# Optimization experiments

Hardware: AMD Instinct MI355X
Metric: run time of the kernel (lower is better)

## Reference

```python
import jax, jax.numpy as jnp
import numpy as np

LN_EPS = 1e-5

def setup_inputs() -> dict:
    key = jax.random.key(0)
    ks = jax.random.split(key, 12)
    B, S, M, C, D = 16, 1024, 4096, 768, 256
    inp = {
        'seed_xyz_norm': jax.random.normal(ks[0], (B, S, 3), jnp.float32),
        'p_last': jax.random.normal(ks[1], (B, M, 3), jnp.float32),
        'f_last': jax.random.normal(ks[2], (B, C, M), jnp.float32),
        'seed_features': jax.random.normal(ks[3], (B, D, S), jnp.float32),
        # LayerNorm params over C
        'ln_gamma': jnp.ones((C,), jnp.float32),
        'ln_beta': jnp.zeros((C,), jnp.float32),
        # conv1d projector C -> 256 (kernel size 1) + ReLU
        'proj_w': jax.random.normal(ks[4], (D, C), jnp.float32) * (1.0 / np.sqrt(C)),
        'proj_b': jnp.zeros((D,), jnp.float32),
        # fusion MLP: concat512 -> 512 -> 256 (1x1 convs)
        'mlp_w1': jax.random.normal(ks[5], (2 * D, 2 * D), jnp.float32) * (1.0 / np.sqrt(2 * D)),
        'mlp_b1': jnp.zeros((2 * D,), jnp.float32),
        'mlp_w2': jax.random.normal(ks[6], (D, 2 * D), jnp.float32) * (1.0 / np.sqrt(2 * D)),
        'mlp_b2': jnp.zeros((D,), jnp.float32),
    }
    return inp


def reference(seed_xyz_norm, p_last, f_last, seed_features,
              ln_gamma, ln_beta, proj_w, proj_b,
              mlp_w1, mlp_b1, mlp_w2, mlp_b2):
    # --- nearest_neighbor_gather_features ---
    # squared distance [B,S,M]; argmin over M, gather features [B,C,S]
    d2 = jnp.sum(seed_xyz_norm * seed_xyz_norm, -1, keepdims=True) \
         - 2.0 * jnp.einsum('bsd,bmd->bsm', seed_xyz_norm, p_last) \
         + jnp.sum(p_last * p_last, -1)[:, None, :]
    idx = jnp.argmin(d2, axis=-1)                                   # [B,S]
    lift3d_raw = jnp.take_along_axis(f_last, idx[:, None, :], axis=2)  # [B,C,S]

    # --- LayerNorm over channel dim C ---
    mu = jnp.mean(lift3d_raw, axis=1, keepdims=True)
    var = jnp.mean((lift3d_raw - mu) ** 2, axis=1, keepdims=True)
    x_ln = (lift3d_raw - mu) * jax.lax.rsqrt(var + LN_EPS)
    x_ln = x_ln * ln_gamma[None, :, None] + ln_beta[None, :, None]

    # --- conv1d projector (1x1) + ReLU ---
    proj = jax.nn.relu(jnp.einsum('oc,bcs->bos', proj_w, x_ln) + proj_b[None, :, None])

    # --- concat fusion MLP ---
    fused = jnp.concatenate([seed_features, proj], axis=1)          # [B,512,S]
    h = jax.nn.relu(jnp.einsum('oc,bcs->bos', mlp_w1, fused) + mlp_b1[None, :, None])
    mixed = jnp.einsum('oc,bcs->bos', mlp_w2, h) + mlp_b2[None, :, None]  # [B,256,S]
    return mixed
```

## Files before the change

### kernel.cpp

```cpp
#include <hip/hip_runtime.h>

namespace {

constexpr int B = 16, S = 1024, M = 4096, C = 768, D = 256;

typedef __attribute__((ext_vector_type(8))) short bf16x8;
typedef __attribute__((ext_vector_type(4))) float f32x4;

__device__ inline ushort f2bf(float f) {
  uint u = __float_as_uint(f);
  uint r = (u + 0x7FFFu + ((u >> 16) & 1u)) >> 16;
  return (ushort)r;
}

__global__ __launch_bounds__(256)
void nn_kernel(const float* __restrict__ xyz, const float* __restrict__ p,
               int* __restrict__ idx_out) {
  const int b = blockIdx.y;
  const int t = threadIdx.x;
  const int seed = blockIdx.x * 16 + (t >> 4);
  const int l16 = t & 15;

  const float sx = xyz[((size_t)b * S + seed) * 3 + 0];
  const float sy = xyz[((size_t)b * S + seed) * 3 + 1];
  const float sz = xyz[((size_t)b * S + seed) * 3 + 2];
  const float ss = __fadd_rn(__fadd_rn(__fmul_rn(sx, sx), __fmul_rn(sy, sy)),
                             __fmul_rn(sz, sz));

  __shared__ float4 pt[256];

  float best = 3.4028235e38f;
  int besti = 0;
  const float* pb = p + (size_t)b * M * 3;

  for (int m0 = 0; m0 < M; m0 += 256) {
    __syncthreads();
    {
      const float a0 = pb[(size_t)(m0 + t) * 3 + 0];
      const float a1 = pb[(size_t)(m0 + t) * 3 + 1];
      const float a2 = pb[(size_t)(m0 + t) * 3 + 2];
      const float pp = __fadd_rn(__fadd_rn(__fmul_rn(a0, a0), __fmul_rn(a1, a1)),
                                 __fmul_rn(a2, a2));
      pt[t] = make_float4(a0, a1, a2, pp);
    }
    __syncthreads();
    #pragma unroll 4
    for (int j = l16; j < 256; j += 16) {
      const float4 q = pt[j];
      float dot = __fmul_rn(sx, q.x);
      dot = __fadd_rn(dot, __fmul_rn(sy, q.y));
      dot = __fadd_rn(dot, __fmul_rn(sz, q.z));
      const float d2 = __fadd_rn(__fsub_rn(ss, __fmul_rn(2.0f, dot)), q.w);
      const int mi = m0 + j;
      if (d2 < best || (d2 == best && mi < besti)) { best = d2; besti = mi; }
    }
  }
  #pragma unroll
  for (int off = 8; off >= 1; off >>= 1) {
    const float ob = __shfl_xor(best, off, 16);
    const int   oi = __shfl_xor(besti, off, 16);
    if (ob < best || (ob == best && oi < besti)) { best = ob; besti = oi; }
  }
  if (l16 == 0) idx_out[b * S + seed] = besti;
}

__global__ __launch_bounds__(256)
void bucket_sort_kernel(const int* __restrict__ idx, int* __restrict__ sIdx,
                        int* __restrict__ sS) {
  const int b = blockIdx.x;
  const int t = threadIdx.x;
  __shared__ int keys[1024];
  __shared__ int cnt[256];
  __shared__ int base[256];
  __shared__ int wsum[4];

  cnt[t] = 0;
  #pragma unroll
  for (int i = 0; i < 4; ++i) keys[t + 256 * i] = idx[b * S + t + 256 * i];
  __syncthreads();
  #pragma unroll
  for (int i = 0; i < 4; ++i) atomicAdd(&cnt[keys[t + 256 * i] >> 4], 1);
  __syncthreads();

  const int v = cnt[t];
  int sc = v;
  #pragma unroll
  for (int off = 1; off < 64; off <<= 1) {
    const int o = __shfl_up(sc, off);
    if ((t & 63) >= off) sc += o;
  }
  if ((t & 63) == 63) wsum[t >> 6] = sc;
  __syncthreads();
  int wb = 0;
  #pragma unroll
  for (int w = 0; w < 4; ++w)
    if (w < (t >> 6)) wb += wsum[w];
  base[t] = wb + sc - v;
  cnt[t] = 0;
  __syncthreads();

  #pragma unroll
  for (int i = 0; i < 4; ++i) {
    const int s = t + 256 * i;
    const int m = keys[s];
    const int bu = m >> 4;
    const int r = base[bu] + atomicAdd(&cnt[bu], 1);
    sIdx[b * S + r] = m;
    sS[b * S + r] = s;
  }
}

__global__ __launch_bounds__(256)
void gather_ln_kernel(const float* __restrict__ f, const int* __restrict__ sIdx,
                      const int* __restrict__ sS,
                      const float* __restrict__ gamma, const float* __restrict__ beta,
                      ushort* __restrict__ xln) {
  const int b = blockIdx.y;
  const int rl = blockIdx.x;
  const int r0 = (((rl & 7) << 5) + (rl >> 3)) << 2;
  const int t = threadIdx.x;

  int sR[4], mR[4];
  #pragma unroll
  for (int i = 0; i < 4; ++i) {
    sR[i] = sS[b * S + r0 + i];
    mR[i] = sIdx[b * S + r0 + i];
  }

  const float* fb = f + (size_t)b * C * M;
  float v[4][3];
  #pragma unroll
  for (int i = 0; i < 4; ++i) {
    v[i][0] = fb[(size_t)(t      ) * M + mR[i]];
    v[i][1] = fb[(size_t)(t + 256) * M + mR[i]];
    v[i][2] = fb[(size_t)(t + 512) * M + mR[i]];
  }

  const float g0 = gamma[t], g1 = gamma[t + 256], g2 = gamma[t + 512];
  const float e0 = beta[t],  e1 = beta[t + 256],  e2 = beta[t + 512];

  __shared__ float red[4][4];
  __shared__ float stats[8];
  const int wave = t >> 6;

  float ps[4];
  #pragma unroll
  for (int i = 0; i < 4; ++i) ps[i] = v[i][0] + v[i][1] + v[i][2];
  #pragma unroll
  for (int off = 32; off >= 1; off >>= 1) {
    #pragma unroll
    for (int i = 0; i < 4; ++i) ps[i] += __shfl_xor(ps[i], off);
  }
  if ((t & 63) == 0) {
    #pragma unroll
    for (int i = 0; i < 4; ++i) red[i][wave] = ps[i];
  }
  __syncthreads();
  if (t < 4)
    stats[t] = (red[t][0] + red[t][1] + red[t][2] + red[t][3]) * (1.0f / 768.0f);
  __syncthreads();

  float d[4][3];
  #pragma unroll
  for (int i = 0; i < 4; ++i) {
    const float mu = stats[i];
    d[i][0] = v[i][0] - mu; d[i][1] = v[i][1] - mu; d[i][2] = v[i][2] - mu;
  }
  float pv[4];
  #pragma unroll
  for (int i = 0; i < 4; ++i)
    pv[i] = d[i][0] * d[i][0] + d[i][1] * d[i][1] + d[i][2] * d[i][2];
  #pragma unroll
  for (int off = 32; off >= 1; off >>= 1) {
    #pragma unroll
    for (int i = 0; i < 4; ++i) pv[i] += __shfl_xor(pv[i], off);
  }
  if ((t & 63) == 0) {
    #pragma unroll
    for (int i = 0; i < 4; ++i) red[i][wave] = pv[i];
  }
  __syncthreads();
  if (t < 4) {
    const float var = (red[t][0] + red[t][1] + red[t][2] + red[t][3]) * (1.0f / 768.0f);
    stats[4 + t] = 1.0f / sqrtf(var + 1e-5f);
  }
  __syncthreads();

  #pragma unroll
  for (int i = 0; i < 4; ++i) {
    const float rs = stats[4 + i];
    ushort* o = xln + ((size_t)b * S + sR[i]) * C;
    o[t      ] = f2bf((d[i][0] * rs) * g0 + e0);
    o[t + 256] = f2bf((d[i][1] * rs) * g1 + e1);
    o[t + 512] = f2bf((d[i][2] * rs) * g2 + e2);
  }
}

__global__ __launch_bounds__(256)
void prep_kernel(const float* __restrict__ sf, ushort* __restrict__ fused,
                 const float* __restrict__ w0, int n0, ushort* __restrict__ o0,
                 const float* __restrict__ w1, int n1, ushort* __restrict__ o1,
                 const float* __restrict__ w2, int n2, ushort* __restrict__ o2) {
  __shared__ float tile[64][68];
  const int bid = blockIdx.x;
  const int t = threadIdx.x;

  if (bid < 1024) {
    const int b  = bid >> 6;
    const int d0 = ((bid >> 4) & 3) * 64;
    const int s0 = (bid & 15) * 64;

    const float* inb = sf + ((size_t)b * D + d0) * S + s0;
    #pragma unroll
    for (int q = 0; q < 4; ++q) {
      const int rr = (t >> 4) + q * 16;
      const int c4 = (t & 15) * 4;
      const float4 v = *(const float4*)&inb[(size_t)rr * S + c4];
      *(float4*)&tile[rr][c4] = v;
    }
    __syncthreads();
    #pragma unroll
    for (int q = 0; q < 4; ++q) {
      const int srow = (t >> 4) + q * 16;
      const int dc = (t & 15) * 4;
      ushort4 o;
      o.x = f2bf(tile[dc + 0][srow]);
      o.y = f2bf(tile[dc + 1][srow]);
      o.z = f2bf(tile[dc + 2][srow]);
      o.w = f2bf(tile[dc + 3][srow]);
      *(ushort4*)&fused[((size_t)b * S + s0 + srow) * 512 + d0 + dc] = o;
    }
  } else {
    const int id = bid - 1024;
    const int which = id >> 8;
    const float* src = which == 0 ? w0 : which == 1 ? w1 : w2;
    ushort* dst = which == 0 ? o0 : which == 1 ? o1 : o2;
    const int n = which == 0 ? n0 : which == 1 ? n1 : n2;
    const int i = ((id & 255) * 256 + t) * 4;
    if (i < n) {
      const float4 v = *(const float4*)&src[i];
      ushort4 o;
      o.x = f2bf(v.x); o.y = f2bf(v.y); o.z = f2bf(v.z); o.w = f2bf(v.w);
      *(ushort4*)&dst[i] = o;
    }
  }
}

__global__ __launch_bounds__(256)
void gemm_bf16_kernel(const ushort* __restrict__ W, int K, int O,
                      const ushort* __restrict__ X,
                      const float* __restrict__ bias,
                      void* __restrict__ out, int outMode, int ldOut, int colOff,
                      int relu) {
  const int b  = blockIdx.z;
  const int s0 = blockIdx.x * 128;
  const int o0 = blockIdx.y * 128;
  const int t  = threadIdx.x;
  const int wave = t >> 6;
  const int lane = t & 63;
  const int l16 = lane & 15;
  const int quad = lane >> 4;

  __shared__ ushort Wt[2][128 * 40];
  __shared__ ushort Xt[2][128 * 40];
  __shared__ float biasS[128];

  if (t < 128) biasS[t] = bias[o0 + t];

  f32x4 acc[8][2];
  const f32x4 z = {0.f, 0.f, 0.f, 0.f};
  #pragma unroll
  for (int of = 0; of < 8; ++of) { acc[of][0] = z; acc[of][1] = z; }

  const ushort* Xb = X + (size_t)b * S * K;
  const int kg = t & 3;
  const int row = t >> 2;
  const size_t wBase = (size_t)(o0 + row) * K + kg * 8;
  const size_t xBase = (size_t)(s0 + row) * K + kg * 8;
  const size_t wBase2 = wBase + (size_t)64 * K;
  const size_t xBase2 = xBase + (size_t)64 * K;
  const int T = K >> 5;

  uint4 wv0 = *(const uint4*)&W[wBase];
  uint4 wv1 = *(const uint4*)&W[wBase2];
  uint4 xv0 = *(const uint4*)&Xb[xBase];
  uint4 xv1 = *(const uint4*)&Xb[xBase2];
  *(uint4*)&Wt[0][row * 40 + kg * 8] = wv0;
  *(uint4*)&Wt[0][(row + 64) * 40 + kg * 8] = wv1;
  *(uint4*)&Xt[0][row * 40 + kg * 8] = xv0;
  *(uint4*)&Xt[0][(row + 64) * 40 + kg * 8] = xv1;
  if (T > 1) {
    wv0 = *(const uint4*)&W[wBase + 32];
    wv1 = *(const uint4*)&W[wBase2 + 32];
    xv0 = *(const uint4*)&Xb[xBase + 32];
    xv1 = *(const uint4*)&Xb[xBase2 + 32];
  }
  __syncthreads();

  for (int tt = 0; tt < T; ++tt) {
    const int cur = tt & 1;

    if (tt + 1 < T) {
      *(uint4*)&Wt[cur ^ 1][row * 40 + kg * 8] = wv0;
      *(uint4*)&Wt[cur ^ 1][(row + 64) * 40 + kg * 8] = wv1;
      *(uint4*)&Xt[cur ^ 1][row * 40 + kg * 8] = xv0;
      *(uint4*)&Xt[cur ^ 1][(row + 64) * 40 + kg * 8] = xv1;
    }
    if (tt + 2 < T) {
      const int c = (tt + 2) * 32;
      wv0 = *(const uint4*)&W[wBase + c];
      wv1 = *(const uint4*)&W[wBase2 + c];
      xv0 = *(const uint4*)&Xb[xBase + c];
      xv1 = *(const uint4*)&Xb[xBase2 + c];
    }
    bf16x8 bfr[2];
    #pragma unroll
    for (int sf = 0; sf < 2; ++sf)
      bfr[sf] = *(const bf16x8*)&Xt[cur][(wave * 32 + sf * 16 + l16) * 40 + quad * 8];
    #pragma unroll
    for (int of = 0; of < 8; ++of) {
      const bf16x8 afr = *(const bf16x8*)&Wt[cur][(of * 16 + l16) * 40 + quad * 8];
      acc[of][0] = __builtin_amdgcn_mfma_f32_16x16x32_bf16(afr, bfr[0], acc[of][0], 0, 0, 0);
      acc[of][1] = __builtin_amdgcn_mfma_f32_16x16x32_bf16(afr, bfr[1], acc[of][1], 0, 0, 0);
    }
    __syncthreads();
  }

  if (outMode == 0) {
    ushort* ob = (ushort*)out;
    #pragma unroll
    for (int of = 0; of < 8; ++of) {
      #pragma unroll
      for (int sf = 0; sf < 2; ++sf) {
        const int s = s0 + wave * 32 + sf * 16 + l16;
        const int ol = of * 16 + quad * 4;
        float v0 = acc[of][sf].x + biasS[ol + 0];
        float v1 = acc[of][sf].y + biasS[ol + 1];
        float v2 = acc[of][sf].z + biasS[ol + 2];
        float v3 = acc[of][sf].w + biasS[ol + 3];
        if (relu) {
          v0 = fmaxf(v0, 0.f); v1 = fmaxf(v1, 0.f);
          v2 = fmaxf(v2, 0.f); v3 = fmaxf(v3, 0.f);
        }
        ushort4 st;
        st.x = f2bf(v0); st.y = f2bf(v1); st.z = f2bf(v2); st.w = f2bf(v3);
        *(ushort4*)&ob[((size_t)b * S + s) * ldOut + colOff + o0 + ol] = st;
      }
    }
  } else {
    float* o32 = (float*)out;
    #pragma unroll
    for (int of = 0; of < 8; ++of) {
      #pragma unroll
      for (int sf = 0; sf < 2; ++sf) {
        const int s = s0 + wave * 32 + sf * 16 + l16;
        const int ol = of * 16 + quad * 4;
        const float vr[4] = {acc[of][sf].x, acc[of][sf].y, acc[of][sf].z, acc[of][sf].w};
        #pragma unroll
        for (int r = 0; r < 4; ++r) {
          const int o = o0 + ol + r;
          o32[((size_t)b * O + o) * S + s] = vr[r] + biasS[ol + r];
        }
      }
    }
  }
}

}

extern "C" void kernel_launch(void* const* d_in, const int* in_sizes, int n_in,
                              void* d_out, int out_size, void* d_ws, size_t ws_size,
                              hipStream_t stream) {
  const float* seed_xyz  = (const float*)d_in[0];
  const float* p_last    = (const float*)d_in[1];
  const float* f_last    = (const float*)d_in[2];
  const float* seed_feat = (const float*)d_in[3];
  const float* ln_gamma  = (const float*)d_in[4];
  const float* ln_beta   = (const float*)d_in[5];
  const float* proj_w    = (const float*)d_in[6];
  const float* proj_b    = (const float*)d_in[7];
  const float* mlp_w1    = (const float*)d_in[8];
  const float* mlp_b1    = (const float*)d_in[9];
  const float* mlp_w2    = (const float*)d_in[10];
  const float* mlp_b2    = (const float*)d_in[11];
  float* out = (float*)d_out;

  char* ws = (char*)d_ws;
  int*    idx   = (int*)(ws);
  int*    sIdx  = (int*)(ws + (64 << 10));
  int*    sS    = (int*)(ws + (128 << 10));
  ushort* wp_bf = (ushort*)(ws + (256 << 10));
  ushort* w1_bf = (ushort*)(ws + (640 << 10));
  ushort* w2_bf = (ushort*)(ws + (1152 << 10));
  ushort* xln   = (ushort*)(ws + (2ull << 20));
  ushort* fused = (ushort*)(ws + (26ull << 20));
  ushort* hbuf  = (ushort*)(ws + (42ull << 20));

  nn_kernel<<<dim3(S / 16, B), 256, 0, stream>>>(seed_xyz, p_last, idx);
  bucket_sort_kernel<<<dim3(B), 256, 0, stream>>>(idx, sIdx, sS);

  gather_ln_kernel<<<dim3(S / 4, B), 256, 0, stream>>>(f_last, sIdx, sS,
                                                       ln_gamma, ln_beta, xln);

  prep_kernel<<<dim3(1024 + 768), 256, 0, stream>>>(
      seed_feat, fused,
      proj_w, D * C, wp_bf, mlp_w1, 512 * 512, w1_bf, mlp_w2, 256 * 512, w2_bf);

  gemm_bf16_kernel<<<dim3(S / 128, 256 / 128, B), 256, 0, stream>>>(
      wp_bf, C, 256, xln, proj_b, fused, 0, 512, 256, 1);

  gemm_bf16_kernel<<<dim3(S / 128, 512 / 128, B), 256, 0, stream>>>(
      w1_bf, 512, 512, fused, mlp_b1, hbuf, 0, 512, 0, 1);

  gemm_bf16_kernel<<<dim3(S / 128, 256 / 128, B), 256, 0, stream>>>(
      w2_bf, 512, 256, hbuf, mlp_b2, out, 1, 0, 0, 0);
}
```

Measured before the change: 409.1 us.

## Reshape GEMM tiles to 256x64 with single-buffered LDS staging

Changes the bf16 GEMM block tile from 128 outputs x 128 seeds to 256 outputs x 64 seeds, with each wave owning 16 seeds across all 256 output channels. The double-buffered LDS scheme is replaced by a single buffer guarded by two barriers per K-step, with register prefetch of the next slice. The aim is to cut LDS footprint and reuse each X fragment across 16 MFMAs, at the cost of an extra barrier per step and less overlap between LDS writes and compute. The grid also changes shape, giving more blocks along the seed dimension.

```diff
diff --git a/kernel.cpp b/kernel.cpp
--- a/kernel.cpp
+++ b/kernel.cpp
@@ -253,114 +253,88 @@
                       void* __restrict__ out, int outMode, int ldOut, int colOff,
                       int relu) {
   const int b  = blockIdx.z;
-  const int s0 = blockIdx.x * 128;
-  const int o0 = blockIdx.y * 128;
+  const int s0 = blockIdx.x * 64;
+  const int o0 = blockIdx.y * 256;
   const int t  = threadIdx.x;
   const int wave = t >> 6;
   const int lane = t & 63;
   const int l16 = lane & 15;
   const int quad = lane >> 4;
 
-  __shared__ ushort Wt[2][128 * 40];
-  __shared__ ushort Xt[2][128 * 40];
-  __shared__ float biasS[128];
-
-  if (t < 128) biasS[t] = bias[o0 + t];
-
-  f32x4 acc[8][2];
+  __shared__ ushort Wt[256 * 40];
+  __shared__ ushort Xt[64 * 40];
+  __shared__ float biasS[256];
+
+  biasS[t] = bias[o0 + t];
+
+  f32x4 acc[16];
   const f32x4 z = {0.f, 0.f, 0.f, 0.f};
   #pragma unroll
-  for (int of = 0; of < 8; ++of) { acc[of][0] = z; acc[of][1] = z; }
+  for (int of = 0; of < 16; ++of) acc[of] = z;
 
   const ushort* Xb = X + (size_t)b * S * K;
   const int kg = t & 3;
   const int row = t >> 2;
   const size_t wBase = (size_t)(o0 + row) * K + kg * 8;
   const size_t xBase = (size_t)(s0 + row) * K + kg * 8;
-  const size_t wBase2 = wBase + (size_t)64 * K;
-  const size_t xBase2 = xBase + (size_t)64 * K;
-  const int T = K >> 5;
-
-  uint4 wv0 = *(const uint4*)&W[wBase];
-  uint4 wv1 = *(const uint4*)&W[wBase2];
-  uint4 xv0 = *(const uint4*)&Xb[xBase];
-  uint4 xv1 = *(const uint4*)&Xb[xBase2];
-  *(uint4*)&Wt[0][row * 40 + kg * 8] = wv0;
-  *(uint4*)&Wt[0][(row + 64) * 40 + kg * 8] = wv1;
-  *(uint4*)&Xt[0][row * 40 + kg * 8] = xv0;
-  *(uint4*)&Xt[0][(row + 64) * 40 + kg * 8] = xv1;
-  if (T > 1) {
-    wv0 = *(const uint4*)&W[wBase + 32];
-    wv1 = *(const uint4*)&W[wBase2 + 32];
-    xv0 = *(const uint4*)&Xb[xBase + 32];
-    xv1 = *(const uint4*)&Xb[xBase2 + 32];
-  }
-  __syncthreads();
-
-  for (int tt = 0; tt < T; ++tt) {
-    const int cur = tt & 1;
-
-    if (tt + 1 < T) {
-      *(uint4*)&Wt[cur ^ 1][row * 40 + kg * 8] = wv0;
-      *(uint4*)&Wt[cur ^ 1][(row + 64) * 40 + kg * 8] = wv1;
-      *(uint4*)&Xt[cur ^ 1][row * 40 + kg * 8] = xv0;
-      *(uint4*)&Xt[cur ^ 1][(row + 64) * 40 + kg * 8] = xv1;
-    }
-    if (tt + 2 < T) {
-      const int c = (tt + 2) * 32;
-      wv0 = *(const uint4*)&W[wBase + c];
-      wv1 = *(const uint4*)&W[wBase2 + c];
-      xv0 = *(const uint4*)&Xb[xBase + c];
-      xv1 = *(const uint4*)&Xb[xBase2 + c];
-    }
-    bf16x8 bfr[2];
-    #pragma unroll
-    for (int sf = 0; sf < 2; ++sf)
-      bfr[sf] = *(const bf16x8*)&Xt[cur][(wave * 32 + sf * 16 + l16) * 40 + quad * 8];
-    #pragma unroll
-    for (int of = 0; of < 8; ++of) {
-      const bf16x8 afr = *(const bf16x8*)&Wt[cur][(of * 16 + l16) * 40 + quad * 8];
-      acc[of][0] = __builtin_amdgcn_mfma_f32_16x16x32_bf16(afr, bfr[0], acc[of][0], 0, 0, 0);
-      acc[of][1] = __builtin_amdgcn_mfma_f32_16x16x32_bf16(afr, bfr[1], acc[of][1], 0, 0, 0);
-    }
-    __syncthreads();
-  }
-
+
+  uint4 wv[4], xv;
+  #pragma unroll
+  for (int q = 0; q < 4; ++q)
+    wv[q] = *(const uint4*)&W[wBase + (size_t)(64 * q) * K];
+  xv = *(const uint4*)&Xb[xBase];
+
+  for (int c0 = 0; c0 < K; c0 += 32) {
+    __syncthreads();
+    #pragma unroll
+    for (int q = 0; q < 4; ++q)
+      *(uint4*)&Wt[(row + 64 * q) * 40 + kg * 8] = wv[q];
+    *(uint4*)&Xt[row * 40 + kg * 8] = xv;
+    __syncthreads();
+
+    if (c0 + 32 < K) {
+      #pragma unroll
+      for (int q = 0; q < 4; ++q)
+        wv[q] = *(const uint4*)&W[wBase + (size_t)(64 * q) * K + c0 + 32];
+      xv = *(const uint4*)&Xb[xBase + c0 + 32];
+    }
+
+    const bf16x8 bfr = *(const bf16x8*)&Xt[(wave * 16 + l16) * 40 + quad * 8];
+    #pragma unroll
+    for (int of = 0; of < 16; ++of) {
+      const bf16x8 afr = *(const bf16x8*)&Wt[(of * 16 + l16) * 40 + quad * 8];
+      acc[of] = __builtin_amdgcn_mfma_f32_16x16x32_bf16(afr, bfr, acc[of], 0, 0, 0);
+    }
+  }
+
+  const int s = s0 + wave * 16 + l16;
   if (outMode == 0) {
     ushort* ob = (ushort*)out;
     #pragma unroll
-    for (int of = 0; of < 8; ++of) {
-      #pragma unroll
-      for (int sf = 0; sf < 2; ++sf) {
-        const int s = s0 + wave * 32 + sf * 16 + l16;
-        const int ol = of * 16 + quad * 4;
-        float v0 = acc[of][sf].x + biasS[ol + 0];
-        float v1 = acc[of][sf].y + biasS[ol + 1];
-        float v2 = acc[of][sf].z + biasS[ol + 2];
-        float v3 = acc[of][sf].w + biasS[ol + 3];
-        if (relu) {
-          v0 = fmaxf(v0, 0.f); v1 = fmaxf(v1, 0.f);
-          v2 = fmaxf(v2, 0.f); v3 = fmaxf(v3, 0.f);
-        }
-        ushort4 st;
-        st.x = f2bf(v0); st.y = f2bf(v1); st.z = f2bf(v2); st.w = f2bf(v3);
-        *(ushort4*)&ob[((size_t)b * S + s) * ldOut + colOff + o0 + ol] = st;
+    for (int of = 0; of < 16; ++of) {
+      const int ol = of * 16 + quad * 4;
+      float v0 = acc[of].x + biasS[ol + 0];
+      float v1 = acc[of].y + biasS[ol + 1];
+      float v2 = acc[of].z + biasS[ol + 2];
+      float v3 = acc[of].w + biasS[ol + 3];
+      if (relu) {
+        v0 = fmaxf(v0, 0.f); v1 = fmaxf(v1, 0.f);
+        v2 = fmaxf(v2, 0.f); v3 = fmaxf(v3, 0.f);
       }
+      ushort4 st;
+      st.x = f2bf(v0); st.y = f2bf(v1); st.z = f2bf(v2); st.w = f2bf(v3);
+      *(ushort4*)&ob[((size_t)b * S + s) * ldOut + colOff + o0 + ol] = st;
     }
   } else {
     float* o32 = (float*)out;
     #pragma unroll
-    for (int of = 0; of < 8; ++of) {
+    for (int of = 0; of < 16; ++of) {
+      const int ol = of * 16 + quad * 4;
+      const float vr[4] = {acc[of].x, acc[of].y, acc[of].z, acc[of].w};
       #pragma unroll
-      for (int sf = 0; sf < 2; ++sf) {
-        const int s = s0 + wave * 32 + sf * 16 + l16;
-        const int ol = of * 16 + quad * 4;
-        const float vr[4] = {acc[of][sf].x, acc[of][sf].y, acc[of][sf].z, acc[of][sf].w};
-        #pragma unroll
-        for (int r = 0; r < 4; ++r) {
-          const int o = o0 + ol + r;
-          o32[((size_t)b * O + o) * S + s] = vr[r] + biasS[ol + r];
-        }
+      for (int r = 0; r < 4; ++r) {
+        const int o = o0 + ol + r;
+        o32[((size_t)b * O + o) * S + s] = vr[r] + biasS[ol + r];
       }
     }
   }
@@ -406,12 +380,12 @@
       seed_feat, fused,
       proj_w, D * C, wp_bf, mlp_w1, 512 * 512, w1_bf, mlp_w2, 256 * 512, w2_bf);
 
-  gemm_bf16_kernel<<<dim3(S / 128, 256 / 128, B), 256, 0, stream>>>(
+  gemm_bf16_kernel<<<dim3(S / 64, 256 / 256, B), 256, 0, stream>>>(
       wp_bf, C, 256, xln, proj_b, fused, 0, 512, 256, 1);
 
-  gemm_bf16_kernel<<<dim3(S / 128, 512 / 128, B), 256, 0, stream>>>(
+  gemm_bf16_kernel<<<dim3(S / 64, 512 / 256, B), 256, 0, stream>>>(
       w1_bf, 512, 512, fused, mlp_b1, hbuf, 0, 512, 0, 1);
 
-  gemm_bf16_kernel<<<dim3(S / 128, 256 / 128, B), 256, 0, stream>>>(
+  gemm_bf16_kernel<<<dim3(S / 64, 256 / 256, B), 256, 0, stream>>>(
       w2_bf, 512, 256, hbuf, mlp_b2, out, 1, 0, 0, 0);
 }
```

Result: slower. 482.5 us (+18.0%).
